# Optimization experiments

Hardware: AMD Instinct MI355X
Metric: run time of the kernel (lower is better)

The kernel has to match this reference:

```python
import jax, jax.numpy as jnp
import numpy as np

B, N = 1, 4096
D_IN, D_OUT, H = 256, 256, 8
HD = D_OUT // H
NEG = -9e15


def _xavier(key, shape):
    lim = np.sqrt(6.0 / (shape[0] + shape[1])).astype(np.float32)
    return jax.random.uniform(key, shape, jnp.float32, -lim, lim)


def setup_inputs() -> dict:
    key = jax.random.key(0)
    ks = jax.random.split(key, 8)
    x = jax.random.normal(ks[0], (B, N, D_IN), jnp.float32)
    adj = (jax.random.uniform(ks[1], (B, N, N)) < 0.05).astype(jnp.float32)
    idx = jnp.arange(N)
    adj = adj.at[:, idx, idx].set(1.0)
    Wq = _xavier(ks[2], (D_IN, D_OUT)); bq = jnp.zeros((D_OUT,), jnp.float32)
    Wk = _xavier(ks[3], (D_IN, D_OUT)); bk = jnp.zeros((D_OUT,), jnp.float32)
    Wv = _xavier(ks[4], (D_IN, D_OUT)); bv = jnp.zeros((D_OUT,), jnp.float32)
    Wo = _xavier(ks[5], (D_OUT, D_OUT)); bo = jnp.zeros((D_OUT,), jnp.float32)
    return dict(x=x, adj=adj, Wq=Wq, bq=bq, Wk=Wk, bk=bk, Wv=Wv, bv=bv, Wo=Wo, bo=bo)


def reference(x, adj, Wq, bq, Wk, bk, Wv, bv, Wo, bo):
    b, n, _ = x.shape
    def split_heads(t):  # [B,N,D_OUT] -> [B,H,N,HD]
        return t.reshape(b, n, H, HD).transpose(0, 2, 1, 3)
    q = split_heads(x @ Wq + bq)
    k = split_heads(x @ Wk + bk)
    v = split_heads(x @ Wv + bv)
    scores = jnp.einsum('bhqd,bhkd->bhqk', q, k) / np.float32(np.sqrt(HD))
    scores = jnp.where(adj[:, None, :, :] > 0, scores, jnp.float32(NEG))
    attn = jax.nn.softmax(scores, axis=-1)
    # dropout is identity in eval mode (training=False)
    out = jnp.einsum('bhqk,bhkd->bhqd', attn, v)
    out = out.transpose(0, 2, 1, 3).reshape(b, n, D_OUT)
    return out @ Wo + bo
```

## Files before the change

kernel.cpp:

```cpp
#include <hip/hip_runtime.h>
#include <hip/hip_bf16.h>
#include <stdint.h>

#define NTOK 4096
#define DIM  256
#define NH   8
#define HD   32
#define MAXNNZ 512

typedef __attribute__((ext_vector_type(8))) short short8;
typedef __attribute__((ext_vector_type(4))) float float4v;
typedef __attribute__((ext_vector_type(2))) float f32x2;
typedef __attribute__((ext_vector_type(2))) _Float16 h2;
typedef unsigned short u16;
typedef unsigned int u32;

__device__ __forceinline__ float bf2f(u16 u) {
    union { u32 u; float f; } c; c.u = ((u32)u) << 16; return c.f;
}
__device__ __forceinline__ u16 f2bf(float f) {
    union { float f; u32 u; } c; c.f = f;
    u32 u = c.u;
    u = u + 0x7FFFu + ((u >> 16) & 1u);
    return (u16)(u >> 16);
}
__device__ __forceinline__ u16 f2h(float f) {
    union { _Float16 h; u16 u; } c; c.h = (_Float16)f; return c.u;
}
__device__ __forceinline__ h2 bch2(u32 v) {
    union { u32 u; h2 h; } c; c.u = v; return c.h;
}
__device__ __forceinline__ float blo(u32 c) {
    union { u32 u; float f; } x; x.u = c << 16; return x.f;
}
__device__ __forceinline__ float bhi(u32 c) {
    union { u32 u; float f; } x; x.u = c & 0xFFFF0000u; return x.f;
}
__device__ __forceinline__ float qsum4(float s) {
    union { float f; int i; } c, r;
    c.f = s;
    r.i = __builtin_amdgcn_mov_dpp(c.i, 0xB1, 0xF, 0xF, true);
    c.f += r.f;
    r.i = __builtin_amdgcn_mov_dpp(c.i, 0x4E, 0xF, 0xF, true);
    return c.f + r.f;
}

__global__ void x_to_bf16(const float* __restrict__ x, u16* __restrict__ xb) {
    int i = (blockIdx.x * blockDim.x + threadIdx.x) * 4;
    float4 v = *(const float4*)(x + i);
    ushort4 o;
    o.x = f2bf(v.x); o.y = f2bf(v.y); o.z = f2bf(v.z); o.w = f2bf(v.w);
    *(ushort4*)(xb + i) = o;
}

__global__ void transpose_w(const float* __restrict__ Wq, const float* __restrict__ Wk,
                            const float* __restrict__ Wv, const float* __restrict__ Wo,
                            u16* __restrict__ WT) {
    const float* srcs[4] = {Wq, Wk, Wv, Wo};
    const float* W = srcs[blockIdx.y];
    int o = blockIdx.x, i = threadIdx.x;
    WT[blockIdx.y * 65536 + o * 256 + i] = f2bf(W[i * 256 + o]);
}

__global__ __launch_bounds__(256) void adj_to_list(const float* __restrict__ adj,
                                                   u16* __restrict__ NL,
                                                   u32* __restrict__ NC) {
    __shared__ u32 cnt;
    int row = blockIdx.x, t = threadIdx.x;
    if (t == 0) cnt = 0;
    __syncthreads();
    const float4* rp = (const float4*)(adj + (size_t)row * NTOK);
    u16* lbase = NL + (size_t)row * MAXNNZ;
#pragma unroll
    for (int i = 0; i < 4; ++i) {
        float4 v = rp[i * 256 + t];
        u32 m = 0;
        if (v.x != 0.f) m |= 1u;
        if (v.y != 0.f) m |= 2u;
        if (v.z != 0.f) m |= 4u;
        if (v.w != 0.f) m |= 8u;
        if (m) {
            int p = __popc(m);
            u32 base = atomicAdd(&cnt, (u32)p);
            int col0 = (i * 256 + t) * 4;
            while (m) {
                int j = __builtin_ctz(m);
                m &= m - 1;
                if (base < MAXNNZ) lbase[base] = (u16)(col0 + j);
                ++base;
            }
        }
    }
    __syncthreads();
    if (t == 0) NC[row] = (cnt < MAXNNZ) ? cnt : MAXNNZ;
}

__global__ __launch_bounds__(64) void qkv_gemm(
    const u16* __restrict__ xb,
    const u16* __restrict__ WT,
    const float* __restrict__ bq, const float* __restrict__ bk, const float* __restrict__ bv,
    u16* __restrict__ Q, u16* __restrict__ K, u16* __restrict__ V) {
    int lane = threadIdx.x, quad = lane >> 4, l16 = lane & 15;
    int mtile = blockIdx.x, ntile = blockIdx.y, mat = blockIdx.z;
    const float* bias = (mat == 0) ? bq : (mat == 1) ? bk : bv;
    const u16* arow = xb + (size_t)(mtile * 16 + l16) * DIM + quad * 8;
    const u16* brow = WT + (size_t)mat * 65536 + (size_t)(ntile * 16 + l16) * DIM + quad * 8;
    float4v acc = {0.f, 0.f, 0.f, 0.f};
#pragma unroll
    for (int k0 = 0; k0 < DIM; k0 += 32) {
        short8 af = *(const short8*)(arow + k0);
        short8 bf = *(const short8*)(brow + k0);
        acc = __builtin_amdgcn_mfma_f32_16x16x32_bf16(af, bf, acc, 0, 0, 0);
    }
    int n = ntile * 16 + l16;
    float bb = bias[n];
    const float sc = (mat == 0) ? 0.25503635559913516f : 1.0f;
    u16* dst = (mat == 0) ? Q : (mat == 1) ? K : V;
#pragma unroll
    for (int r = 0; r < 4; ++r) {
        int m = mtile * 16 + quad * 4 + r;
        float y = (acc[r] + bb) * sc;
        dst[(size_t)m * DIM + n] = (mat == 2) ? f2bf(y) : f2h(y);
    }
}

__global__ __launch_bounds__(256, 4) void sparse_attn(
    const u16* __restrict__ Q, const u16* __restrict__ K, const u16* __restrict__ V,
    const u16* __restrict__ NL, const u32* __restrict__ NC,
    u16* __restrict__ AO) {
    __shared__ float part[2][32][9];
    int tid  = threadIdx.x;
    int rb   = __builtin_amdgcn_readfirstlane(tid >> 7);
    int half = __builtin_amdgcn_readfirstlane((tid >> 6) & 1);
    int lane = tid & 63;
    int p = lane >> 5;
    int t = lane & 31;
    int row = __builtin_amdgcn_readfirstlane((int)blockIdx.x * 2 + rb);
    int pshift = p << 4;
    u32 tOff = (u32)(t * 8);

    uint4 qq = *(const uint4*)(Q + (size_t)row * DIM + t * 8);
    h2 qh0 = bch2(qq.x), qh1 = bch2(qq.y), qh2 = bch2(qq.z), qh3 = bch2(qq.w);

    f32x2 O0 = {0.f, 0.f}, O1 = {0.f, 0.f}, O2 = {0.f, 0.f}, O3 = {0.f, 0.f};
    float lsum = 0.f;

    int nnz = __builtin_amdgcn_readfirstlane((int)NC[row]);
    const u16* lst = NL + (size_t)row * MAXNNZ;
    int nh    = ((nnz + 4) >> 3) << 2;
    int begin = half ? nh : 0;
    int end   = half ? nnz : nh;

#define BODY(kk, vv, EVALID)                                                     \
    {                                                                            \
        float a = __builtin_amdgcn_fdot2(bch2(kk.x), qh0, 0.f, false);           \
        float b = __builtin_amdgcn_fdot2(bch2(kk.y), qh1, 0.f, false);           \
        a = __builtin_amdgcn_fdot2(bch2(kk.z), qh2, a, false);                   \
        b = __builtin_amdgcn_fdot2(bch2(kk.w), qh3, b, false);                   \
        float s = qsum4(a + b);             \
        float e = __builtin_amdgcn_exp2f(s);                                     \
        if (!(EVALID)) e = 0.f;                 \
        lsum += e;                                                               \
        f32x2 ev = {e, e};                                                       \
        O0 = __builtin_elementwise_fma(ev, (f32x2){blo(vv.x), bhi(vv.x)}, O0);   \
        O1 = __builtin_elementwise_fma(ev, (f32x2){blo(vv.y), bhi(vv.y)}, O1);   \
        O2 = __builtin_elementwise_fma(ev, (f32x2){blo(vv.z), bhi(vv.z)}, O2);   \
        O3 = __builtin_elementwise_fma(ev, (f32x2){blo(vv.w), bhi(vv.w)}, O3);   \
    }

    int n = begin;
    bool haveFull = (begin + 4 <= end);
    if (haveFull) {
        u32 wA = *(const u32*)(lst + begin);
        u32 wB = *(const u32*)(lst + begin + 2);
        u32 offA = (((wA >> pshift) & 0xFFFFu) << 8) + tOff;
        u32 offB = (((wB >> pshift) & 0xFFFFu) << 8) + tOff;
        uint4 kA = *(const uint4*)(K + offA);
        uint4 vA = *(const uint4*)(V + offA);
        uint4 kB = *(const uint4*)(K + offB);
        uint4 vB = *(const uint4*)(V + offB);
        u32 wNA = *(const u32*)(lst + begin + 4);
        u32 wNB = *(const u32*)(lst + begin + 6);
        for (; n + 8 <= end; n += 4) {
            u32 offAn = (((wNA >> pshift) & 0xFFFFu) << 8) + tOff;
            u32 offBn = (((wNB >> pshift) & 0xFFFFu) << 8) + tOff;
            uint4 kAn = *(const uint4*)(K + offAn);
            uint4 vAn = *(const uint4*)(V + offAn);
            uint4 kBn = *(const uint4*)(K + offBn);
            uint4 vBn = *(const uint4*)(V + offBn);
            wNA = *(const u32*)(lst + n + 8);
            wNB = *(const u32*)(lst + n + 10);
            BODY(kA, vA, true)
            BODY(kB, vB, true)
            kA = kAn; vA = vAn; kB = kBn; vB = vBn;
        }
        BODY(kA, vA, true)
        BODY(kB, vB, true)
        n += 4;
    }
    if (n < end) {
        u32 wA = *(const u32*)(lst + n);
        u32 wB = *(const u32*)(lst + n + 2);
        u32 lo = wA & 0xFFFFu;
        bool mA = (n + p) < end;
        bool mB = (n + 2 + p) < end;
        u32 idxA = mA ? ((wA >> pshift) & 0xFFFFu) : lo;
        u32 idxB = mB ? ((wB >> pshift) & 0xFFFFu) : lo;
        u32 offA = (idxA << 8) + tOff;
        u32 offB = (idxB << 8) + tOff;
        uint4 kT  = *(const uint4*)(K + offA);
        uint4 vT  = *(const uint4*)(V + offA);
        uint4 kT2 = *(const uint4*)(K + offB);
        uint4 vT2 = *(const uint4*)(V + offB);
        BODY(kT, vT, mA)
        BODY(kT2, vT2, mB)
    }
#undef BODY

    float Of[8] = {O0.x, O0.y, O1.x, O1.y, O2.x, O2.y, O3.x, O3.y};
#pragma unroll
    for (int i = 0; i < 8; ++i) Of[i] += __shfl_xor(Of[i], 32, 64);
    lsum += __shfl_xor(lsum, 32, 64);

    if (half == 1 && p == 0) {
#pragma unroll
        for (int i = 0; i < 8; ++i) part[rb][t][i] = Of[i];
        part[rb][t][8] = lsum;
    }
    __syncthreads();
    if (half == 0 && p == 0) {
#pragma unroll
        for (int i = 0; i < 8; ++i) Of[i] += part[rb][t][i];
        lsum += part[rb][t][8];
        float inv = 1.0f / lsum;
        u32 w0 = (u32)f2bf(Of[0] * inv) | ((u32)f2bf(Of[1] * inv) << 16);
        u32 w1 = (u32)f2bf(Of[2] * inv) | ((u32)f2bf(Of[3] * inv) << 16);
        u32 w2 = (u32)f2bf(Of[4] * inv) | ((u32)f2bf(Of[5] * inv) << 16);
        u32 w3 = (u32)f2bf(Of[6] * inv) | ((u32)f2bf(Of[7] * inv) << 16);
        *(uint4*)(AO + (size_t)row * DIM + t * 8) = make_uint4(w0, w1, w2, w3);
    }
}

__global__ __launch_bounds__(64) void out_gemm(
    const u16* __restrict__ AO, const u16* __restrict__ WTo, const float* __restrict__ bo,
    float* __restrict__ out) {
    int lane = threadIdx.x, quad = lane >> 4, l16 = lane & 15;
    int mtile = blockIdx.x, ntile = blockIdx.y;
    const u16* arow = AO + (size_t)(mtile * 16 + l16) * DIM + quad * 8;
    const u16* brow = WTo + (size_t)(ntile * 16 + l16) * DIM + quad * 8;
    float4v acc = {0.f, 0.f, 0.f, 0.f};
#pragma unroll
    for (int k0 = 0; k0 < DIM; k0 += 32) {
        short8 af = *(const short8*)(arow + k0);
        short8 bf = *(const short8*)(brow + k0);
        acc = __builtin_amdgcn_mfma_f32_16x16x32_bf16(af, bf, acc, 0, 0, 0);
    }
    int n = ntile * 16 + l16;
    float bb = bo[n];
#pragma unroll
    for (int r = 0; r < 4; ++r)
        out[(size_t)(mtile * 16 + quad * 4 + r) * DIM + n] = acc[r] + bb;
}

extern "C" void kernel_launch(void* const* d_in, const int* in_sizes, int n_in,
                              void* d_out, int out_size, void* d_ws, size_t ws_size,
                              hipStream_t stream) {
    const float* x   = (const float*)d_in[0];
    const float* adj = (const float*)d_in[1];
    const float* Wq  = (const float*)d_in[2];
    const float* bq  = (const float*)d_in[3];
    const float* Wk  = (const float*)d_in[4];
    const float* bk  = (const float*)d_in[5];
    const float* Wv  = (const float*)d_in[6];
    const float* bv  = (const float*)d_in[7];
    const float* Wo  = (const float*)d_in[8];
    const float* bo  = (const float*)d_in[9];

    char* ws = (char*)d_ws;
    const size_t MB = 1u << 20;
    u16* Q   = (u16*)(ws);
    u16* K   = (u16*)(ws + 2 * MB);
    u16* V   = (u16*)(ws + 4 * MB);
    u16* AO  = (u16*)(ws + 6 * MB);
    u16* WT  = (u16*)(ws + 8 * MB);
    u16* XB  = (u16*)(ws + 8 * MB + 512 * 1024);
    u16* NL  = (u16*)(ws + 11 * MB);
    u32* NC  = (u32*)(ws + 15 * MB);

    x_to_bf16<<<dim3(1024), 256, 0, stream>>>(x, XB);
    transpose_w<<<dim3(256, 4), 256, 0, stream>>>(Wq, Wk, Wv, Wo, WT);
    adj_to_list<<<dim3(4096), 256, 0, stream>>>(adj, NL, NC);
    qkv_gemm<<<dim3(256, 16, 3), 64, 0, stream>>>(XB, WT, bq, bk, bv, Q, K, V);
    sparse_attn<<<dim3(2048), 256, 0, stream>>>(Q, K, V, NL, NC, AO);
    out_gemm<<<dim3(256, 16), 64, 0, stream>>>(AO, WT + 3 * 65536, bo, (float*)d_out);
}
```

Baseline: 192.2 us.

## Merge prep kernels into one launch and use wave ballots for adjacency compaction

```diff
diff --git a/kernel.cpp b/kernel.cpp
--- a/kernel.cpp
+++ b/kernel.cpp
@@ -14,6 +14,7 @@
 typedef __attribute__((ext_vector_type(2))) _Float16 h2;
 typedef unsigned short u16;
 typedef unsigned int u32;
+typedef unsigned long long u64;
 
 __device__ __forceinline__ float bf2f(u16 u) {
     union { u32 u; float f; } c; c.u = ((u32)u) << 16; return c.f;
@@ -45,54 +46,60 @@
     return c.f + r.f;
 }
 
-__global__ void x_to_bf16(const float* __restrict__ x, u16* __restrict__ xb) {
-    int i = (blockIdx.x * blockDim.x + threadIdx.x) * 4;
-    float4 v = *(const float4*)(x + i);
-    ushort4 o;
-    o.x = f2bf(v.x); o.y = f2bf(v.y); o.z = f2bf(v.z); o.w = f2bf(v.w);
-    *(ushort4*)(xb + i) = o;
-}
-
-__global__ void transpose_w(const float* __restrict__ Wq, const float* __restrict__ Wk,
-                            const float* __restrict__ Wv, const float* __restrict__ Wo,
-                            u16* __restrict__ WT) {
-    const float* srcs[4] = {Wq, Wk, Wv, Wo};
-    const float* W = srcs[blockIdx.y];
-    int o = blockIdx.x, i = threadIdx.x;
-    WT[blockIdx.y * 65536 + o * 256 + i] = f2bf(W[i * 256 + o]);
-}
-
-__global__ __launch_bounds__(256) void adj_to_list(const float* __restrict__ adj,
-                                                   u16* __restrict__ NL,
-                                                   u32* __restrict__ NC) {
+__global__ __launch_bounds__(256) void prep(
+    const float* __restrict__ x,
+    const float* __restrict__ Wq, const float* __restrict__ Wk,
+    const float* __restrict__ Wv, const float* __restrict__ Wo,
+    const float* __restrict__ adj,
+    u16* __restrict__ xb, u16* __restrict__ WT,
+    u16* __restrict__ NL, u32* __restrict__ NC) {
+    int b = blockIdx.x, t = threadIdx.x;
+    if (b >= NTOK) {
+        int m = b - NTOK;
+        if (m < 1024) {
+            int i = (m * 256 + t) * 4;
+            float4 v = *(const float4*)(x + i);
+            ushort4 o;
+            o.x = f2bf(v.x); o.y = f2bf(v.y); o.z = f2bf(v.z); o.w = f2bf(v.w);
+            *(ushort4*)(xb + i) = o;
+        } else {
+            m -= 1024;
+            const float* srcs[4] = {Wq, Wk, Wv, Wo};
+            int mat = m >> 8, o = m & 255;
+            WT[mat * 65536 + o * 256 + t] = f2bf(srcs[mat][t * 256 + o]);
+        }
+        return;
+    }
     __shared__ u32 cnt;
-    int row = blockIdx.x, t = threadIdx.x;
     if (t == 0) cnt = 0;
     __syncthreads();
-    const float4* rp = (const float4*)(adj + (size_t)row * NTOK);
-    u16* lbase = NL + (size_t)row * MAXNNZ;
+    int lane = t & 63;
+    u64 below = ((u64)1 << lane) - 1;
+    const float4* rp = (const float4*)(adj + (size_t)b * NTOK);
+    u16* lbase = NL + (size_t)b * MAXNNZ;
 #pragma unroll
     for (int i = 0; i < 4; ++i) {
         float4 v = rp[i * 256 + t];
-        u32 m = 0;
-        if (v.x != 0.f) m |= 1u;
-        if (v.y != 0.f) m |= 2u;
-        if (v.z != 0.f) m |= 4u;
-        if (v.w != 0.f) m |= 8u;
-        if (m) {
-            int p = __popc(m);
-            u32 base = atomicAdd(&cnt, (u32)p);
-            int col0 = (i * 256 + t) * 4;
-            while (m) {
-                int j = __builtin_ctz(m);
-                m &= m - 1;
-                if (base < MAXNNZ) lbase[base] = (u16)(col0 + j);
-                ++base;
-            }
-        }
+        bool px = v.x != 0.f, py = v.y != 0.f, pz = v.z != 0.f, pw = v.w != 0.f;
+        u64 bx = __ballot(px), by = __ballot(py);
+        u64 bz = __ballot(pz), bw = __ballot(pw);
+        u32 cx = __popcll(bx), cy = __popcll(by), cz = __popcll(bz);
+        u32 total = cx + cy + cz + __popcll(bw);
+        u32 wbase = 0;
+        if (lane == 0 && total) wbase = atomicAdd(&cnt, total);
+        wbase = __shfl(wbase, 0, 64);
+        int col0 = (i * 256 + t) * 4;
+        u32 ox = wbase + __popcll(bx & below);
+        u32 oy = wbase + cx + __popcll(by & below);
+        u32 oz = wbase + cx + cy + __popcll(bz & below);
+        u32 ow = wbase + cx + cy + cz + __popcll(bw & below);
+        if (px && ox < MAXNNZ) lbase[ox] = (u16)(col0 + 0);
+        if (py && oy < MAXNNZ) lbase[oy] = (u16)(col0 + 1);
+        if (pz && oz < MAXNNZ) lbase[oz] = (u16)(col0 + 2);
+        if (pw && ow < MAXNNZ) lbase[ow] = (u16)(col0 + 3);
     }
     __syncthreads();
-    if (t == 0) NC[row] = (cnt < MAXNNZ) ? cnt : MAXNNZ;
+    if (t == 0) NC[b] = (cnt < MAXNNZ) ? cnt : MAXNNZ;
 }
 
 __global__ __launch_bounds__(64) void qkv_gemm(
@@ -287,9 +294,8 @@
     u16* NL  = (u16*)(ws + 11 * MB);
     u32* NC  = (u32*)(ws + 15 * MB);
 
-    x_to_bf16<<<dim3(1024), 256, 0, stream>>>(x, XB);
-    transpose_w<<<dim3(256, 4), 256, 0, stream>>>(Wq, Wk, Wv, Wo, WT);
-    adj_to_list<<<dim3(4096), 256, 0, stream>>>(adj, NL, NC);
+    prep<<<dim3(NTOK + 1024 + 1024), 256, 0, stream>>>(
+        x, Wq, Wk, Wv, Wo, adj, XB, WT, NL, NC);
     qkv_gemm<<<dim3(256, 16, 3), 64, 0, stream>>>(XB, WT, bq, bk, bv, Q, K, V);
     sparse_attn<<<dim3(2048), 256, 0, stream>>>(Q, K, V, NL, NC, AO);
     out_gemm<<<dim3(256, 16), 64, 0, stream>>>(AO, WT + 3 * 65536, bo, (float*)d_out);
```

New measurement: 181.1 us. 5.8% less time.
